# Performance work log

Hardware: AMD Instinct MI355X
Metric: run time of the kernel (lower is better)

The kernel has to match this reference:

```python
import jax, jax.numpy as jnp
import numpy as np

B, S, D = 4, 2048, 1024
E, TOP_K = 8, 2
N_FF = 4096
H = int(2 * N_FF / 3)  # 2730, Expert hidden when ffn_multiplier is None


def setup_inputs() -> dict:
    key = jax.random.key(0)
    ks = jax.random.split(key, 8)
    s = 0.02
    return {
        "x": jax.random.normal(ks[0], (B, S, D), jnp.float32),
        "noise": jax.random.normal(ks[1], (B, S, E), jnp.float32),
        "w_route": jax.random.normal(ks[2], (D, E), jnp.float32) * s,
        "b_route": jnp.zeros((E,), jnp.float32),
        "w_noise": jax.random.normal(ks[3], (D, E), jnp.float32) * s,
        "b_noise": jnp.zeros((E,), jnp.float32),
        "w_proj": jax.random.normal(ks[4], (E, D, 2 * H), jnp.float32) * s,  # SwiGLU proj per expert
        "w_down": jax.random.normal(ks[5], (E, H, D), jnp.float32) * s,
    }


def reference(x, noise, w_route, b_route, w_noise, b_noise, w_proj, w_down):
    b, s, d = x.shape
    e = w_route.shape[1]
    n = b * s
    capacity = int(n * TOP_K / e * 1.0)  # capacity_factor = 1.0

    # --- NoisyTopkRouter (temperature = 1.0) ---
    logits = jnp.einsum("bsd,de->bse", x, w_route) + b_route
    noise_scale = jax.nn.softplus(jnp.einsum("bsd,de->bse", x, w_noise) + b_noise)
    noisy = logits + noise * noise_scale
    top_v, top_i = jax.lax.top_k(noisy, TOP_K)  # [b,s,k]
    # softmax over -inf-filled sparse logits == softmax over the top-k values,
    # scattered back to the expert axis
    probs_k = jax.nn.softmax(top_v, axis=-1)  # [b,s,k]
    routing = jnp.sum(jax.nn.one_hot(top_i, e, dtype=x.dtype) * probs_k[..., None], axis=-2)  # [b,s,e]
    router_prob = routing.mean(axis=(0, 1))
    aux_loss = jnp.sum((router_prob - 1.0 / e) ** 2)

    # --- dispatch ---
    flat_x = x.reshape(n, d)
    flat_gate = routing.reshape(n, e)
    hit = jnp.any(top_i.reshape(n, TOP_K)[:, :, None] == jnp.arange(e)[None, None, :], axis=1)  # [n,e]

    def per_expert(mask_e, gate_e, wp, wd):
        # keep first `capacity` selected tokens, in token order (matches torch nonzero order)
        keep = mask_e & (jnp.cumsum(mask_e) <= capacity)
        sel = jnp.argsort(~keep, stable=True)[:capacity]  # selected token ids first, in order
        valid = keep[sel].astype(flat_x.dtype)
        xin = flat_x[sel]  # [capacity, d]
        x1, x2 = jnp.split(xin @ wp, 2, axis=-1)
        out = (jax.nn.silu(x1) * x2) @ wd  # [capacity, d]
        w = gate_e[sel] * valid
        return sel, out * w[:, None]

    sel, contrib = jax.vmap(per_expert)(hit.T, flat_gate.T, w_proj, w_down)  # [e,cap], [e,cap,d]
    updates = jnp.zeros_like(flat_x).at[sel.reshape(-1)].add(contrib.reshape(-1, d))
    return updates.reshape(b, s, d), aux_loss
```

## Files before the change

### kernel.cpp

```cpp
#include <hip/hip_runtime.h>
#include <cstdint>
#include <cstddef>

#define NTOK 8192
#define DMODEL 1024
#define NEXP 8
#define CAP 2048
#define HFF 2730
#define HFF2 5460
#define KPAD 2752

typedef float f32x4 __attribute__((ext_vector_type(4)));
typedef __attribute__((ext_vector_type(8))) short short8;

__device__ inline unsigned short f2bf(float f) {
  union { float f; unsigned u; } v; v.f = f;
  unsigned u = v.u;
  return (unsigned short)((u + 0x7FFFu + ((u >> 16) & 1u)) >> 16);
}
__device__ inline float bf2f(unsigned short s) {
  union { unsigned u; float f; } v; v.u = ((unsigned)s) << 16; return v.f;
}

typedef __attribute__((address_space(1))) const void g_void;
typedef __attribute__((address_space(3))) void l_void;
__device__ __forceinline__ void dma16(const void* g, void* l) {
  __builtin_amdgcn_global_load_lds((g_void*)g, (l_void*)l, 16, 0, 0);
}

__global__ void cast_x_kernel(const float* __restrict__ x, unsigned short* __restrict__ xb) {
  size_t i = ((size_t)blockIdx.x * 256 + threadIdx.x) * 8;
  float4 v0 = *(const float4*)(x + i);
  float4 v1 = *(const float4*)(x + i + 4);
  union { short8 v; unsigned short s[8]; } p;
  p.s[0] = f2bf(v0.x); p.s[1] = f2bf(v0.y); p.s[2] = f2bf(v0.z); p.s[3] = f2bf(v0.w);
  p.s[4] = f2bf(v1.x); p.s[5] = f2bf(v1.y); p.s[6] = f2bf(v1.z); p.s[7] = f2bf(v1.w);
  *(short8*)(xb + i) = p.v;
}

__global__ void router_kernel(const float* __restrict__ x,
                              const float* __restrict__ noise,
                              const float* __restrict__ w_route,
                              const float* __restrict__ b_route,
                              const float* __restrict__ w_noise,
                              const float* __restrict__ b_noise,
                              int* __restrict__ topi,
                              float* __restrict__ gates) {
  const int lane = threadIdx.x & 63;
  const int wave = threadIdx.x >> 6;
  const int tok = blockIdx.x * 4 + wave;
  const float* xr = x + (size_t)tok * DMODEL;

  double aR[8], aN[8];
#pragma unroll
  for (int e = 0; e < 8; e++) { aR[e] = 0.0; aN[e] = 0.0; }

  for (int d = lane; d < DMODEL; d += 64) {
    double xv = (double)xr[d];
    const float* wr = w_route + d * 8;
    const float* wn = w_noise + d * 8;
#pragma unroll
    for (int e = 0; e < 8; e++) {
      aR[e] += xv * (double)wr[e];
      aN[e] += xv * (double)wn[e];
    }
  }
#pragma unroll
  for (int off = 32; off > 0; off >>= 1) {
#pragma unroll
    for (int e = 0; e < 8; e++) {
      aR[e] += __shfl_down(aR[e], (unsigned)off, 64);
      aN[e] += __shfl_down(aN[e], (unsigned)off, 64);
    }
  }
  if (lane == 0) {
    double nv[8];
#pragma unroll
    for (int e = 0; e < 8; e++) {
      double lg = aR[e] + (double)b_route[e];
      double ns = aN[e] + (double)b_noise[e];
      double sp = fmax(ns, 0.0) + log1p(exp(-fabs(ns)));
      nv[e] = lg + (double)noise[(size_t)tok * 8 + e] * sp;
    }
    int i0 = 0;
#pragma unroll
    for (int e = 1; e < 8; e++) if (nv[e] > nv[i0]) i0 = e;
    int i1 = (i0 == 0) ? 1 : 0;
#pragma unroll
    for (int e = 0; e < 8; e++) if (e != i0 && nv[e] > nv[i1]) i1 = e;
    double r = exp(nv[i1] - nv[i0]);
    float g0 = (float)(1.0 / (1.0 + r));
    float g1 = (float)(r / (1.0 + r));
    topi[tok * 2] = i0; topi[tok * 2 + 1] = i1;
    gates[tok * 2] = g0; gates[tok * 2 + 1] = g1;
  }
}

__global__ void aux_kernel(const int* __restrict__ topi,
                           const float* __restrict__ gates,
                           float* __restrict__ out) {
  const int t = threadIdx.x;
  float s[8];
#pragma unroll
  for (int e = 0; e < 8; e++) s[e] = 0.f;
  for (int i = t; i < NTOK; i += 256) {
    int i0 = topi[2 * i], i1 = topi[2 * i + 1];
    float g0 = gates[2 * i], g1 = gates[2 * i + 1];
#pragma unroll
    for (int e = 0; e < 8; e++)
      s[e] += (i0 == e ? g0 : 0.f) + (i1 == e ? g1 : 0.f);
  }
  __shared__ float sh[256][8];
#pragma unroll
  for (int e = 0; e < 8; e++) sh[t][e] = s[e];
  __syncthreads();
  for (int stride = 128; stride > 0; stride >>= 1) {
    if (t < stride) {
#pragma unroll
      for (int e = 0; e < 8; e++) sh[t][e] += sh[t + stride][e];
    }
    __syncthreads();
  }
  if (t == 0) {
    float aux = 0.f;
#pragma unroll
    for (int e = 0; e < 8; e++) {
      float p = sh[0][e] / (float)NTOK - 0.125f;
      aux += p * p;
    }
    out[(size_t)NTOK * DMODEL] = aux;
  }
}

__global__ void dispatch_kernel(const int* __restrict__ topi,
                                const float* __restrict__ gates,
                                int* __restrict__ sel,
                                float* __restrict__ gsel,
                                int* __restrict__ slot) {
  const int e = blockIdx.x;
  const int t = threadIdx.x;
  const int lane = t & 63;
  const int w = t >> 6;
  __shared__ int waveCnt[16];
  __shared__ int runningS;
  if (t == 0) runningS = 0;
  __syncthreads();

  for (int base = 0; base < NTOK; base += 1024) {
    int tok = base + t;
    int i0 = topi[2 * tok], i1 = topi[2 * tok + 1];
    bool hit = (i0 == e) || (i1 == e);
    int kth = (i0 == e) ? 0 : 1;
    float g = gates[2 * tok + kth];
    unsigned long long m = __ballot(hit);
    int prefix = __popcll(m & ((1ull << lane) - 1ull));
    if (lane == 63) waveCnt[w] = prefix + (hit ? 1 : 0);
    __syncthreads();
    int off = runningS;
    for (int ww = 0; ww < w; ww++) off += waveCnt[ww];
    int pos = off + prefix;
    if (hit) {
      if (pos < CAP) {
        sel[e * CAP + pos] = tok; gsel[e * CAP + pos] = g;
        slot[2 * tok + kth] = pos;
      } else {
        slot[2 * tok + kth] = -1;
      }
    }
    __syncthreads();
    if (t == 0) {
      int sacc = 0;
#pragma unroll
      for (int ww = 0; ww < 16; ww++) sacc += waveCnt[ww];
      runningS += sacc;
    }
    __syncthreads();
  }
  for (int p = runningS + t; p < CAP; p += 1024) { sel[e * CAP + p] = 0; gsel[e * CAP + p] = 0.f; }
}

__global__ void transpose_wp_kernel(const float* __restrict__ wp,
                                    unsigned short* __restrict__ wpT) {
  const int e = blockIdx.z, d0 = blockIdx.y * 64, f0 = blockIdx.x * 64;
  __shared__ unsigned short tile[64][68];
  const int t = threadIdx.x;
  const int ld = t >> 4;
  const int lf4 = (t & 15) * 4;
#pragma unroll
  for (int p = 0; p < 4; p++) {
    int d = d0 + p * 16 + ld;
    int f = f0 + lf4;
    if (f < HFF2) {
      float4 v = *(const float4*)(wp + ((size_t)e * DMODEL + d) * HFF2 + f);
      tile[lf4 + 0][p * 16 + ld] = f2bf(v.x);
      tile[lf4 + 1][p * 16 + ld] = f2bf(v.y);
      tile[lf4 + 2][p * 16 + ld] = f2bf(v.z);
      tile[lf4 + 3][p * 16 + ld] = f2bf(v.w);
    }
  }
  __syncthreads();
  const int dq = (t & 7) * 8;
#pragma unroll
  for (int q = 0; q < 2; q++) {
    int fl = q * 32 + (t >> 3);
    int f = f0 + fl;
    if (f < HFF2) {
      ushort4 u0 = *(const ushort4*)&tile[fl][dq];
      ushort4 u1 = *(const ushort4*)&tile[fl][dq + 4];
      union { ushort4 u[2]; short8 v; } pk;
      pk.u[0] = u0; pk.u[1] = u1;
      *(short8*)(wpT + (size_t)e * HFF2 * DMODEL + (size_t)f * DMODEL + d0 + dq) = pk.v;
    }
  }
}

__global__ void transpose_wd_kernel(const float* __restrict__ wd,
                                    unsigned short* __restrict__ wdT) {
  const int e = blockIdx.z, d0 = blockIdx.y * 32, k0 = blockIdx.x * 32;
  __shared__ unsigned short tile[32][33];
  const int t = threadIdx.x;
  {
    int lk = t >> 3, ld4 = (t & 7) * 4;
    int k = k0 + lk;
    if (k < HFF) {
      float4 v = *(const float4*)(wd + (size_t)e * HFF * DMODEL + (size_t)k * DMODEL + d0 + ld4);
      tile[lk][ld4 + 0] = f2bf(v.x);
      tile[lk][ld4 + 1] = f2bf(v.y);
      tile[lk][ld4 + 2] = f2bf(v.z);
      tile[lk][ld4 + 3] = f2bf(v.w);
    } else {
      tile[lk][ld4 + 0] = 0; tile[lk][ld4 + 1] = 0;
      tile[lk][ld4 + 2] = 0; tile[lk][ld4 + 3] = 0;
    }
  }
  __syncthreads();
  {
    int ld = t >> 3, lkq = (t & 7) * 4;
    ushort4 o = make_ushort4(tile[lkq + 0][ld], tile[lkq + 1][ld],
                             tile[lkq + 2][ld], tile[lkq + 3][ld]);
    *(ushort4*)(wdT + (size_t)e * DMODEL * KPAD + (size_t)(d0 + ld) * KPAD + k0 + lkq) = o;
  }
}

__global__ __launch_bounds__(512, 2)
void gemm1_kernel(const unsigned short* __restrict__ xb,
                  const unsigned short* __restrict__ wpT,
                  const int* __restrict__ sel,
                  unsigned short* __restrict__ h) {
  const int e = blockIdx.z;
  const int m0 = blockIdx.x * 256;
  const int n0 = blockIdx.y * 128;

  __shared__ __align__(16) unsigned short smem[4 * 16384];

  const int t = threadIdx.x;
  const int lane = t & 63;
  const int w = t >> 6;
  const int wr = w >> 2;
  const int wc = w & 3;
  const int fr = lane & 15;
  const int fq = lane >> 4;
  const int csw = (fq ^ ((fr >> 1) & 3)) * 8;

  const int r0 = t >> 2;
  const int sw = ((t & 3) ^ ((t >> 3) & 3)) * 8;
  const int tok0 = sel[e * CAP + m0 + r0];
  const int tok1 = sel[e * CAP + m0 + 128 + r0];
  const unsigned short* ga0 = xb + (size_t)tok0 * DMODEL + sw;
  const unsigned short* ga1 = xb + (size_t)tok1 * DMODEL + sw;
  const size_t ebase = (size_t)e * HFF2;
  int c0 = n0 + r0; if (c0 >= HFF) c0 = HFF - 1;
  const unsigned short* gb1 = wpT + (ebase + (size_t)c0) * DMODEL + sw;
  const unsigned short* gb2 = wpT + (ebase + (size_t)(HFF + c0)) * DMODEL + sw;

  const int dOff = w * 1024;

  f32x4 acc1[8][2], acc2[8][2];
#pragma unroll
  for (int i = 0; i < 8; i++)
#pragma unroll
    for (int j = 0; j < 2; j++) { acc1[i][j] = (f32x4)0.f; acc2[i][j] = (f32x4)0.f; }

  auto stageA = [&](int kt) {
    char* b = (char*)smem + (size_t)(kt & 3) * 32768;
    const int k0 = kt * 32;
    dma16(ga0 + k0, b + dOff);
    dma16(ga1 + k0, b + 8192 + dOff);
  };
  auto stageB = [&](int kt) {
    char* b = (char*)smem + (size_t)(kt & 3) * 32768;
    const int k0 = kt * 32;
    dma16(gb1 + k0, b + 16384 + dOff);
    dma16(gb2 + k0, b + 24576 + dOff);
  };

  stageA(0); stageB(0); stageA(1); stageB(1); stageA(2); stageB(2);

  for (int kt = 0; kt < 32; ++kt) {
    if (kt < 30)       asm volatile("s_waitcnt vmcnt(8)" ::: "memory");
    else if (kt == 30) asm volatile("s_waitcnt vmcnt(4)" ::: "memory");
    else               asm volatile("s_waitcnt vmcnt(0)" ::: "memory");
    __builtin_amdgcn_s_barrier();
    asm volatile("" ::: "memory");

    const unsigned short* Ab  = smem + (kt & 3) * 16384;
    const unsigned short* B1b = Ab + 8192;
    const unsigned short* B2b = Ab + 12288;

    short8 a[4], b1[2], b2[2];
#pragma unroll
    for (int i = 0; i < 4; i++)
      a[i] = *(const short8*)(Ab + (wr * 128 + i * 16 + fr) * 32 + csw);
#pragma unroll
    for (int j = 0; j < 2; j++) {
      b1[j] = *(const short8*)(B1b + (wc * 32 + j * 16 + fr) * 32 + csw);
      b2[j] = *(const short8*)(B2b + (wc * 32 + j * 16 + fr) * 32 + csw);
    }
    if (kt < 29) stageA(kt + 3);
    __builtin_amdgcn_s_barrier();
    asm volatile("s_waitcnt lgkmcnt(0)" ::: "memory");
    __builtin_amdgcn_s_setprio(1);
#pragma unroll
    for (int i = 0; i < 4; i++)
#pragma unroll
      for (int j = 0; j < 2; j++) {
        acc1[i][j] = __builtin_amdgcn_mfma_f32_16x16x32_bf16(a[i], b1[j], acc1[i][j], 0, 0, 0);
        acc2[i][j] = __builtin_amdgcn_mfma_f32_16x16x32_bf16(a[i], b2[j], acc2[i][j], 0, 0, 0);
      }
    __builtin_amdgcn_s_setprio(0);
    __builtin_amdgcn_s_barrier();

    short8 a2[4];
#pragma unroll
    for (int i = 0; i < 4; i++)
      a2[i] = *(const short8*)(Ab + (wr * 128 + (i + 4) * 16 + fr) * 32 + csw);
    if (kt < 29) stageB(kt + 3);
    __builtin_amdgcn_s_barrier();
    asm volatile("s_waitcnt lgkmcnt(0)" ::: "memory");
    __builtin_amdgcn_s_setprio(1);
#pragma unroll
    for (int i = 0; i < 4; i++)
#pragma unroll
      for (int j = 0; j < 2; j++) {
        acc1[i + 4][j] = __builtin_amdgcn_mfma_f32_16x16x32_bf16(a2[i], b1[j], acc1[i + 4][j], 0, 0, 0);
        acc2[i + 4][j] = __builtin_amdgcn_mfma_f32_16x16x32_bf16(a2[i], b2[j], acc2[i + 4][j], 0, 0, 0);
      }
    __builtin_amdgcn_s_setprio(0);
  }

#pragma unroll
  for (int i = 0; i < 8; i++) {
#pragma unroll
    for (int j = 0; j < 2; j++) {
      const int col = n0 + wc * 32 + j * 16 + fr;
      if (col < KPAD) {
#pragma unroll
        for (int r = 0; r < 4; r++) {
          const int row = m0 + wr * 128 + i * 16 + fq * 4 + r;
          float v1 = acc1[i][j][r], v2 = acc2[i][j][r];
          float hv = (col < HFF) ? (v1 / (1.f + __expf(-v1))) * v2 : 0.f;
          h[((size_t)e * CAP + row) * KPAD + col] = f2bf(hv);
        }
      }
    }
  }
}

__global__ __launch_bounds__(512, 2)
void gemm2_kernel(const unsigned short* __restrict__ h,
                  const unsigned short* __restrict__ wdT,
                  unsigned short* __restrict__ contrib) {
  const int e = blockIdx.z;
  const int m0 = blockIdx.x * 256;
  const int n0 = blockIdx.y * 256;

  __shared__ __align__(16) unsigned short smem[4 * 16384];

  const int t = threadIdx.x;
  const int lane = t & 63;
  const int w = t >> 6;
  const int wr = w >> 2;
  const int wc = w & 3;
  const int fr = lane & 15;
  const int fq = lane >> 4;
  const int csw = (fq ^ ((fr >> 1) & 3)) * 8;

  const int r0 = t >> 2;
  const int sw = ((t & 3) ^ ((t >> 3) & 3)) * 8;
  const unsigned short* ga0 = h + ((size_t)e * CAP + m0 + r0) * KPAD + sw;
  const unsigned short* ga1 = h + ((size_t)e * CAP + m0 + 128 + r0) * KPAD + sw;
  const unsigned short* gb0 = wdT + ((size_t)e * DMODEL + n0 + r0) * KPAD + sw;
  const unsigned short* gb1 = wdT + ((size_t)e * DMODEL + n0 + 128 + r0) * KPAD + sw;

  const int dOff = w * 1024;

  f32x4 acc[8][4];
#pragma unroll
  for (int i = 0; i < 8; i++)
#pragma unroll
    for (int j = 0; j < 4; j++) acc[i][j] = (f32x4)0.f;

  auto stageA = [&](int kt) {
    char* b = (char*)smem + (size_t)(kt & 3) * 32768;
    const int k0 = kt * 32;
    dma16(ga0 + k0, b + dOff);
    dma16(ga1 + k0, b + 8192 + dOff);
  };
  auto stageB = [&](int kt) {
    char* b = (char*)smem + (size_t)(kt & 3) * 32768;
    const int k0 = kt * 32;
    dma16(gb0 + k0, b + 16384 + dOff);
    dma16(gb1 + k0, b + 24576 + dOff);
  };

  stageA(0); stageB(0); stageA(1); stageB(1); stageA(2); stageB(2);

  for (int kt = 0; kt < 86; ++kt) {
    if (kt < 84)       asm volatile("s_waitcnt vmcnt(8)" ::: "memory");
    else if (kt == 84) asm volatile("s_waitcnt vmcnt(4)" ::: "memory");
    else               asm volatile("s_waitcnt vmcnt(0)" ::: "memory");
    __builtin_amdgcn_s_barrier();
    asm volatile("" ::: "memory");

    const unsigned short* Ab = smem + (kt & 3) * 16384;
    const unsigned short* Bb = Ab + 8192;

    short8 a[4], b[4];
#pragma unroll
    for (int i = 0; i < 4; i++)
      a[i] = *(const short8*)(Ab + (wr * 128 + i * 16 + fr) * 32 + csw);
#pragma unroll
    for (int j = 0; j < 4; j++)
      b[j] = *(const short8*)(Bb + (wc * 64 + j * 16 + fr) * 32 + csw);
    if (kt < 83) stageA(kt + 3);
    __builtin_amdgcn_s_barrier();
    asm volatile("s_waitcnt lgkmcnt(0)" ::: "memory");
    __builtin_amdgcn_s_setprio(1);
#pragma unroll
    for (int i = 0; i < 4; i++)
#pragma unroll
      for (int j = 0; j < 4; j++)
        acc[i][j] = __builtin_amdgcn_mfma_f32_16x16x32_bf16(a[i], b[j], acc[i][j], 0, 0, 0);
    __builtin_amdgcn_s_setprio(0);
    __builtin_amdgcn_s_barrier();

    short8 a2[4];
#pragma unroll
    for (int i = 0; i < 4; i++)
      a2[i] = *(const short8*)(Ab + (wr * 128 + (i + 4) * 16 + fr) * 32 + csw);
    if (kt < 83) stageB(kt + 3);
    __builtin_amdgcn_s_barrier();
    asm volatile("s_waitcnt lgkmcnt(0)" ::: "memory");
    __builtin_amdgcn_s_setprio(1);
#pragma unroll
    for (int i = 0; i < 4; i++)
#pragma unroll
      for (int j = 0; j < 4; j++)
        acc[i + 4][j] = __builtin_amdgcn_mfma_f32_16x16x32_bf16(a2[i], b[j], acc[i + 4][j], 0, 0, 0);
    __builtin_amdgcn_s_setprio(0);
  }

#pragma unroll
  for (int i = 0; i < 8; i++) {
#pragma unroll
    for (int j = 0; j < 4; j++) {
      const int col = n0 + wc * 64 + j * 16 + fr;
#pragma unroll
      for (int r = 0; r < 4; r++) {
        const int row = m0 + wr * 128 + i * 16 + fq * 4 + r;
        contrib[((size_t)e * CAP + row) * DMODEL + col] = f2bf(acc[i][j][r]);
      }
    }
  }
}

__global__ void combine_kernel(const unsigned short* __restrict__ contrib,
                               const int* __restrict__ topi,
                               const int* __restrict__ slot,
                               const float* __restrict__ gates,
                               float* __restrict__ out) {
  const int tok = blockIdx.x;
  const int t = threadIdx.x;
  const int e0 = topi[2 * tok], e1 = topi[2 * tok + 1];
  const int s0 = slot[2 * tok], s1 = slot[2 * tok + 1];
  const float g0 = gates[2 * tok], g1 = gates[2 * tok + 1];
  float4 acc = make_float4(0.f, 0.f, 0.f, 0.f);
  if (s0 >= 0) {
    ushort4 c = *(const ushort4*)(contrib + ((size_t)(e0 * CAP + s0)) * DMODEL + t * 4);
    acc.x += g0 * bf2f(c.x); acc.y += g0 * bf2f(c.y);
    acc.z += g0 * bf2f(c.z); acc.w += g0 * bf2f(c.w);
  }
  if (s1 >= 0) {
    ushort4 c = *(const ushort4*)(contrib + ((size_t)(e1 * CAP + s1)) * DMODEL + t * 4);
    acc.x += g1 * bf2f(c.x); acc.y += g1 * bf2f(c.y);
    acc.z += g1 * bf2f(c.z); acc.w += g1 * bf2f(c.w);
  }
  *(float4*)(out + (size_t)tok * DMODEL + t * 4) = acc;
}

extern "C" void kernel_launch(void* const* d_in, const int* in_sizes, int n_in,
                              void* d_out, int out_size, void* d_ws, size_t ws_size,
                              hipStream_t stream) {
  const float* x = (const float*)d_in[0];
  const float* noise = (const float*)d_in[1];
  const float* w_route = (const float*)d_in[2];
  const float* b_route = (const float*)d_in[3];
  const float* w_noise = (const float*)d_in[4];
  const float* b_noise = (const float*)d_in[5];
  const float* w_proj = (const float*)d_in[6];
  const float* w_down = (const float*)d_in[7];
  float* out = (float*)d_out;

  char* ws = (char*)d_ws;
  const size_t WT_BYTES = (size_t)NEXP * HFF2 * DMODEL * 2;
  const size_t WDT_BYTES = (size_t)NEXP * DMODEL * KPAD * 2;
  const size_t H_BYTES = (size_t)NEXP * CAP * KPAD * 2;
  unsigned short* wT = (unsigned short*)ws;
  unsigned short* contrib = (unsigned short*)(ws + WDT_BYTES);
  unsigned short* hbuf = (unsigned short*)(ws + WT_BYTES);
  char* p = ws + WT_BYTES + H_BYTES;
  int* sel = (int*)p;          p += (size_t)NEXP * CAP * 4;
  float* gsel = (float*)p;     p += (size_t)NEXP * CAP * 4;
  int* topi = (int*)p;         p += (size_t)NTOK * 2 * 4;
  float* gates = (float*)p;    p += (size_t)NTOK * 2 * 4;
  int* slot = (int*)p;

  unsigned short* xb = (unsigned short*)d_out;

  hipLaunchKernelGGL(cast_x_kernel, dim3(NTOK * DMODEL / (256 * 8)), dim3(256), 0, stream, x, xb);
  hipLaunchKernelGGL(router_kernel, dim3(NTOK / 4), dim3(256), 0, stream,
                     x, noise, w_route, b_route, w_noise, b_noise, topi, gates);
  hipLaunchKernelGGL(dispatch_kernel, dim3(NEXP), dim3(1024), 0, stream, topi, gates, sel, gsel, slot);
  hipLaunchKernelGGL(transpose_wp_kernel, dim3(86, 16, NEXP), dim3(256), 0, stream, w_proj, wT);
  hipLaunchKernelGGL(gemm1_kernel, dim3(CAP / 256, 22, NEXP), dim3(512), 0, stream, xb, wT, sel, hbuf);
  hipLaunchKernelGGL(transpose_wd_kernel, dim3(KPAD / 32, DMODEL / 32, NEXP), dim3(256), 0, stream, w_down, wT);
  hipLaunchKernelGGL(gemm2_kernel, dim3(CAP / 256, DMODEL / 256, NEXP), dim3(512), 0, stream,
                     hbuf, wT, contrib);
  hipLaunchKernelGGL(combine_kernel, dim3(NTOK), dim3(256), 0, stream,
                     contrib, topi, slot, gates, out);
  hipLaunchKernelGGL(aux_kernel, dim3(1), dim3(256), 0, stream, topi, gates, out);
}
```

Before: 811.2 us.

## Restructure expert GEMMs into per-wave private LDS tiles without block barriers

Both expert GEMMs now use 4-wave blocks where each wave loads its own A and B fragments into a private double-buffered LDS region. This drops the block-wide barriers and the swizzled shared tiles. Each wave computes a larger 128-row output tile (64x2 columns in gemm1, 128 columns in gemm2), so more MFMAs run per LDS read and synchronization overhead goes down. The cost is that B tiles are no longer shared across waves, which multiplies global/LDS traffic for weights. The unswizzled LDS layout may cause bank conflicts, and the very large accumulator sets (128 and 256 VGPRs of accumulators) with occupancy 1 may spill or hide latency poorly.

```diff
diff --git a/kernel.cpp b/kernel.cpp
--- a/kernel.cpp
+++ b/kernel.cpp
@@ -242,232 +242,179 @@
   }
 }
 
-__global__ __launch_bounds__(512, 2)
+__global__ __launch_bounds__(256, 1)
 void gemm1_kernel(const unsigned short* __restrict__ xb,
                   const unsigned short* __restrict__ wpT,
                   const int* __restrict__ sel,
                   unsigned short* __restrict__ h) {
   const int e = blockIdx.z;
-  const int m0 = blockIdx.x * 256;
-  const int n0 = blockIdx.y * 128;
-
-  __shared__ __align__(16) unsigned short smem[4 * 16384];
+  const int m0 = blockIdx.x * 512;
+  const int n0 = blockIdx.y * 64;
+
+  __shared__ __align__(16) unsigned short smem[65536];
 
   const int t = threadIdx.x;
   const int lane = t & 63;
   const int w = t >> 6;
-  const int wr = w >> 2;
-  const int wc = w & 3;
   const int fr = lane & 15;
   const int fq = lane >> 4;
-  const int csw = (fq ^ ((fr >> 1) & 3)) * 8;
-
-  const int r0 = t >> 2;
-  const int sw = ((t & 3) ^ ((t >> 3) & 3)) * 8;
-  const int tok0 = sel[e * CAP + m0 + r0];
-  const int tok1 = sel[e * CAP + m0 + 128 + r0];
-  const unsigned short* ga0 = xb + (size_t)tok0 * DMODEL + sw;
-  const unsigned short* ga1 = xb + (size_t)tok1 * DMODEL + sw;
-  const size_t ebase = (size_t)e * HFF2;
-  int c0 = n0 + r0; if (c0 >= HFF) c0 = HFF - 1;
-  const unsigned short* gb1 = wpT + (ebase + (size_t)c0) * DMODEL + sw;
-  const unsigned short* gb2 = wpT + (ebase + (size_t)(HFF + c0)) * DMODEL + sw;
-
-  const int dOff = w * 1024;
-
-  f32x4 acc1[8][2], acc2[8][2];
+  const int lr = lane >> 2;
+  const int lk = (lane & 3) * 8;
+
+  const unsigned short* aSrc[8];
+#pragma unroll
+  for (int i = 0; i < 8; i++) {
+    int tok = sel[e * CAP + m0 + w * 128 + i * 16 + lr];
+    aSrc[i] = xb + (size_t)tok * DMODEL + lk;
+  }
+  const unsigned short* bSrc1[4];
+  const unsigned short* bSrc2[4];
+#pragma unroll
+  for (int j = 0; j < 4; j++) {
+    int c = n0 + j * 16 + lr; if (c >= HFF) c = HFF - 1;
+    bSrc1[j] = wpT + ((size_t)e * HFF2 + c) * DMODEL + lk;
+    bSrc2[j] = wpT + ((size_t)e * HFF2 + HFF + c) * DMODEL + lk;
+  }
+  char* myLds = (char*)smem + w * 32768;
+
+  auto stage = [&](int kt) {
+    char* buf = myLds + (kt & 1) * 16384;
+    const int k0 = kt * 32;
+#pragma unroll
+    for (int i = 0; i < 8; i++) dma16(aSrc[i] + k0, buf + i * 1024);
+#pragma unroll
+    for (int j = 0; j < 4; j++) {
+      dma16(bSrc1[j] + k0, buf + 8192 + j * 1024);
+      dma16(bSrc2[j] + k0, buf + 12288 + j * 1024);
+    }
+  };
+
+  f32x4 acc1[8][4], acc2[8][4];
 #pragma unroll
   for (int i = 0; i < 8; i++)
 #pragma unroll
-    for (int j = 0; j < 2; j++) { acc1[i][j] = (f32x4)0.f; acc2[i][j] = (f32x4)0.f; }
-
-  auto stageA = [&](int kt) {
-    char* b = (char*)smem + (size_t)(kt & 3) * 32768;
-    const int k0 = kt * 32;
-    dma16(ga0 + k0, b + dOff);
-    dma16(ga1 + k0, b + 8192 + dOff);
-  };
-  auto stageB = [&](int kt) {
-    char* b = (char*)smem + (size_t)(kt & 3) * 32768;
-    const int k0 = kt * 32;
-    dma16(gb1 + k0, b + 16384 + dOff);
-    dma16(gb2 + k0, b + 24576 + dOff);
-  };
-
-  stageA(0); stageB(0); stageA(1); stageB(1); stageA(2); stageB(2);
+    for (int j = 0; j < 4; j++) { acc1[i][j] = (f32x4)0.f; acc2[i][j] = (f32x4)0.f; }
+
+  stage(0); stage(1);
 
   for (int kt = 0; kt < 32; ++kt) {
-    if (kt < 30)       asm volatile("s_waitcnt vmcnt(8)" ::: "memory");
-    else if (kt == 30) asm volatile("s_waitcnt vmcnt(4)" ::: "memory");
-    else               asm volatile("s_waitcnt vmcnt(0)" ::: "memory");
-    __builtin_amdgcn_s_barrier();
+    if (kt < 31) asm volatile("s_waitcnt vmcnt(16)" ::: "memory");
+    else         asm volatile("s_waitcnt vmcnt(0)" ::: "memory");
     asm volatile("" ::: "memory");
 
-    const unsigned short* Ab  = smem + (kt & 3) * 16384;
-    const unsigned short* B1b = Ab + 8192;
-    const unsigned short* B2b = Ab + 12288;
-
-    short8 a[4], b1[2], b2[2];
-#pragma unroll
-    for (int i = 0; i < 4; i++)
-      a[i] = *(const short8*)(Ab + (wr * 128 + i * 16 + fr) * 32 + csw);
-#pragma unroll
-    for (int j = 0; j < 2; j++) {
-      b1[j] = *(const short8*)(B1b + (wc * 32 + j * 16 + fr) * 32 + csw);
-      b2[j] = *(const short8*)(B2b + (wc * 32 + j * 16 + fr) * 32 + csw);
-    }
-    if (kt < 29) stageA(kt + 3);
-    __builtin_amdgcn_s_barrier();
+    const char* buf = (const char*)myLds + (kt & 1) * 16384;
+    short8 a[8], b1[4], b2[4];
+#pragma unroll
+    for (int i = 0; i < 8; i++)
+      a[i] = *(const short8*)(buf + i * 1024 + fr * 64 + fq * 16);
+#pragma unroll
+    for (int j = 0; j < 4; j++) {
+      b1[j] = *(const short8*)(buf + 8192 + j * 1024 + fr * 64 + fq * 16);
+      b2[j] = *(const short8*)(buf + 12288 + j * 1024 + fr * 64 + fq * 16);
+    }
     asm volatile("s_waitcnt lgkmcnt(0)" ::: "memory");
-    __builtin_amdgcn_s_setprio(1);
-#pragma unroll
-    for (int i = 0; i < 4; i++)
-#pragma unroll
-      for (int j = 0; j < 2; j++) {
+    if (kt < 30) stage(kt + 2);
+#pragma unroll
+    for (int i = 0; i < 8; i++)
+#pragma unroll
+      for (int j = 0; j < 4; j++) {
         acc1[i][j] = __builtin_amdgcn_mfma_f32_16x16x32_bf16(a[i], b1[j], acc1[i][j], 0, 0, 0);
         acc2[i][j] = __builtin_amdgcn_mfma_f32_16x16x32_bf16(a[i], b2[j], acc2[i][j], 0, 0, 0);
       }
-    __builtin_amdgcn_s_setprio(0);
-    __builtin_amdgcn_s_barrier();
-
-    short8 a2[4];
-#pragma unroll
-    for (int i = 0; i < 4; i++)
-      a2[i] = *(const short8*)(Ab + (wr * 128 + (i + 4) * 16 + fr) * 32 + csw);
-    if (kt < 29) stageB(kt + 3);
-    __builtin_amdgcn_s_barrier();
-    asm volatile("s_waitcnt lgkmcnt(0)" ::: "memory");
-    __builtin_amdgcn_s_setprio(1);
-#pragma unroll
-    for (int i = 0; i < 4; i++)
-#pragma unroll
-      for (int j = 0; j < 2; j++) {
-        acc1[i + 4][j] = __builtin_amdgcn_mfma_f32_16x16x32_bf16(a2[i], b1[j], acc1[i + 4][j], 0, 0, 0);
-        acc2[i + 4][j] = __builtin_amdgcn_mfma_f32_16x16x32_bf16(a2[i], b2[j], acc2[i + 4][j], 0, 0, 0);
+  }
+
+#pragma unroll
+  for (int i = 0; i < 8; i++) {
+#pragma unroll
+    for (int j = 0; j < 4; j++) {
+      const int col = n0 + j * 16 + fr;
+#pragma unroll
+      for (int r = 0; r < 4; r++) {
+        const int row = m0 + w * 128 + i * 16 + fq * 4 + r;
+        float v1 = acc1[i][j][r], v2 = acc2[i][j][r];
+        float hv = (col < HFF) ? (v1 / (1.f + __expf(-v1))) * v2 : 0.f;
+        h[((size_t)e * CAP + row) * KPAD + col] = f2bf(hv);
       }
-    __builtin_amdgcn_s_setprio(0);
-  }
-
-#pragma unroll
-  for (int i = 0; i < 8; i++) {
-#pragma unroll
-    for (int j = 0; j < 2; j++) {
-      const int col = n0 + wc * 32 + j * 16 + fr;
-      if (col < KPAD) {
-#pragma unroll
-        for (int r = 0; r < 4; r++) {
-          const int row = m0 + wr * 128 + i * 16 + fq * 4 + r;
-          float v1 = acc1[i][j][r], v2 = acc2[i][j][r];
-          float hv = (col < HFF) ? (v1 / (1.f + __expf(-v1))) * v2 : 0.f;
-          h[((size_t)e * CAP + row) * KPAD + col] = f2bf(hv);
-        }
-      }
-    }
-  }
-}
-
-__global__ __launch_bounds__(512, 2)
+    }
+  }
+}
+
+__global__ __launch_bounds__(256, 1)
 void gemm2_kernel(const unsigned short* __restrict__ h,
                   const unsigned short* __restrict__ wdT,
                   unsigned short* __restrict__ contrib) {
   const int e = blockIdx.z;
-  const int m0 = blockIdx.x * 256;
-  const int n0 = blockIdx.y * 256;
-
-  __shared__ __align__(16) unsigned short smem[4 * 16384];
+  const int m0 = blockIdx.x * 512;
+  const int n0 = blockIdx.y * 128;
+
+  __shared__ __align__(16) unsigned short smem[65536];
 
   const int t = threadIdx.x;
   const int lane = t & 63;
   const int w = t >> 6;
-  const int wr = w >> 2;
-  const int wc = w & 3;
   const int fr = lane & 15;
   const int fq = lane >> 4;
-  const int csw = (fq ^ ((fr >> 1) & 3)) * 8;
-
-  const int r0 = t >> 2;
-  const int sw = ((t & 3) ^ ((t >> 3) & 3)) * 8;
-  const unsigned short* ga0 = h + ((size_t)e * CAP + m0 + r0) * KPAD + sw;
-  const unsigned short* ga1 = h + ((size_t)e * CAP + m0 + 128 + r0) * KPAD + sw;
-  const unsigned short* gb0 = wdT + ((size_t)e * DMODEL + n0 + r0) * KPAD + sw;
-  const unsigned short* gb1 = wdT + ((size_t)e * DMODEL + n0 + 128 + r0) * KPAD + sw;
-
-  const int dOff = w * 1024;
-
-  f32x4 acc[8][4];
+  const int lr = lane >> 2;
+  const int lk = (lane & 3) * 8;
+
+  const unsigned short* aSrc[8];
 #pragma unroll
   for (int i = 0; i < 8; i++)
-#pragma unroll
-    for (int j = 0; j < 4; j++) acc[i][j] = (f32x4)0.f;
-
-  auto stageA = [&](int kt) {
-    char* b = (char*)smem + (size_t)(kt & 3) * 32768;
+    aSrc[i] = h + ((size_t)e * CAP + m0 + w * 128 + i * 16 + lr) * KPAD + lk;
+  const unsigned short* bSrc[8];
+#pragma unroll
+  for (int j = 0; j < 8; j++)
+    bSrc[j] = wdT + ((size_t)e * DMODEL + n0 + j * 16 + lr) * KPAD + lk;
+
+  char* myLds = (char*)smem + w * 32768;
+
+  auto stage = [&](int kt) {
+    char* buf = myLds + (kt & 1) * 16384;
     const int k0 = kt * 32;
-    dma16(ga0 + k0, b + dOff);
-    dma16(ga1 + k0, b + 8192 + dOff);
+#pragma unroll
+    for (int i = 0; i < 8; i++) dma16(aSrc[i] + k0, buf + i * 1024);
+#pragma unroll
+    for (int j = 0; j < 8; j++) dma16(bSrc[j] + k0, buf + 8192 + j * 1024);
   };
-  auto stageB = [&](int kt) {
-    char* b = (char*)smem + (size_t)(kt & 3) * 32768;
-    const int k0 = kt * 32;
-    dma16(gb0 + k0, b + 16384 + dOff);
-    dma16(gb1 + k0, b + 24576 + dOff);
-  };
-
-  stageA(0); stageB(0); stageA(1); stageB(1); stageA(2); stageB(2);
+
+  f32x4 acc[8][8];
+#pragma unroll
+  for (int i = 0; i < 8; i++)
+#pragma unroll
+    for (int j = 0; j < 8; j++) acc[i][j] = (f32x4)0.f;
+
+  stage(0); stage(1);
 
   for (int kt = 0; kt < 86; ++kt) {
-    if (kt < 84)       asm volatile("s_waitcnt vmcnt(8)" ::: "memory");
-    else if (kt == 84) asm volatile("s_waitcnt vmcnt(4)" ::: "memory");
-    else               asm volatile("s_waitcnt vmcnt(0)" ::: "memory");
-    __builtin_amdgcn_s_barrier();
+    if (kt < 85) asm volatile("s_waitcnt vmcnt(16)" ::: "memory");
+    else         asm volatile("s_waitcnt vmcnt(0)" ::: "memory");
     asm volatile("" ::: "memory");
 
-    const unsigned short* Ab = smem + (kt & 3) * 16384;
-    const unsigned short* Bb = Ab + 8192;
-
-    short8 a[4], b[4];
-#pragma unroll
-    for (int i = 0; i < 4; i++)
-      a[i] = *(const short8*)(Ab + (wr * 128 + i * 16 + fr) * 32 + csw);
-#pragma unroll
-    for (int j = 0; j < 4; j++)
-      b[j] = *(const short8*)(Bb + (wc * 64 + j * 16 + fr) * 32 + csw);
-    if (kt < 83) stageA(kt + 3);
-    __builtin_amdgcn_s_barrier();
+    const char* buf = (const char*)myLds + (kt & 1) * 16384;
+    short8 a[8], b[8];
+#pragma unroll
+    for (int i = 0; i < 8; i++)
+      a[i] = *(const short8*)(buf + i * 1024 + fr * 64 + fq * 16);
+#pragma unroll
+    for (int j = 0; j < 8; j++)
+      b[j] = *(const short8*)(buf + 8192 + j * 1024 + fr * 64 + fq * 16);
     asm volatile("s_waitcnt lgkmcnt(0)" ::: "memory");
-    __builtin_amdgcn_s_setprio(1);
-#pragma unroll
-    for (int i = 0; i < 4; i++)
-#pragma unroll
-      for (int j = 0; j < 4; j++)
+    if (kt < 84) stage(kt + 2);
+#pragma unroll
+    for (int i = 0; i < 8; i++)
+#pragma unroll
+      for (int j = 0; j < 8; j++)
         acc[i][j] = __builtin_amdgcn_mfma_f32_16x16x32_bf16(a[i], b[j], acc[i][j], 0, 0, 0);
-    __builtin_amdgcn_s_setprio(0);
-    __builtin_amdgcn_s_barrier();
-
-    short8 a2[4];
-#pragma unroll
-    for (int i = 0; i < 4; i++)
-      a2[i] = *(const short8*)(Ab + (wr * 128 + (i + 4) * 16 + fr) * 32 + csw);
-    if (kt < 83) stageB(kt + 3);
-    __builtin_amdgcn_s_barrier();
-    asm volatile("s_waitcnt lgkmcnt(0)" ::: "memory");
-    __builtin_amdgcn_s_setprio(1);
-#pragma unroll
-    for (int i = 0; i < 4; i++)
-#pragma unroll
-      for (int j = 0; j < 4; j++)
-        acc[i + 4][j] = __builtin_amdgcn_mfma_f32_16x16x32_bf16(a2[i], b[j], acc[i + 4][j], 0, 0, 0);
-    __builtin_amdgcn_s_setprio(0);
   }
 
 #pragma unroll
   for (int i = 0; i < 8; i++) {
 #pragma unroll
-    for (int j = 0; j < 4; j++) {
-      const int col = n0 + wc * 64 + j * 16 + fr;
+    for (int j = 0; j < 8; j++) {
+      const int col = n0 + j * 16 + fr;
 #pragma unroll
       for (int r = 0; r < 4; r++) {
-        const int row = m0 + wr * 128 + i * 16 + fq * 4 + r;
+        const int row = m0 + w * 128 + i * 16 + fq * 4 + r;
         contrib[((size_t)e * CAP + row) * DMODEL + col] = f2bf(acc[i][j][r]);
       }
     }
@@ -532,9 +479,10 @@
                      x, noise, w_route, b_route, w_noise, b_noise, topi, gates);
   hipLaunchKernelGGL(dispatch_kernel, dim3(NEXP), dim3(1024), 0, stream, topi, gates, sel, gsel, slot);
   hipLaunchKernelGGL(transpose_wp_kernel, dim3(86, 16, NEXP), dim3(256), 0, stream, w_proj, wT);
-  hipLaunchKernelGGL(gemm1_kernel, dim3(CAP / 256, 22, NEXP), dim3(512), 0, stream, xb, wT, sel, hbuf);
+  hipLaunchKernelGGL(gemm1_kernel, dim3(CAP / 512, KPAD / 64, NEXP), dim3(256), 0, stream,
+                     xb, wT, sel, hbuf);
   hipLaunchKernelGGL(transpose_wd_kernel, dim3(KPAD / 32, DMODEL / 32, NEXP), dim3(256), 0, stream, w_down, wT);
-  hipLaunchKernelGGL(gemm2_kernel, dim3(CAP / 256, DMODEL / 256, NEXP), dim3(512), 0, stream,
+  hipLaunchKernelGGL(gemm2_kernel, dim3(CAP / 512, DMODEL / 128, NEXP), dim3(256), 0, stream,
                      hbuf, wT, contrib);
   hipLaunchKernelGGL(combine_kernel, dim3(NTOK), dim3(256), 0, stream,
                      contrib, topi, slot, gates, out);
```

Result: slower. 847.1 us (+4.4%).
